# Optimization experiments

Hardware: AMD Instinct MI355X
Metric: run time of the kernel (lower is better)

## Reference

```python
import jax, jax.numpy as jnp
import numpy as np

# Hyperparameters matching the torch module instantiation
STRIDE = (2, 2, 2)
PADDING = (1, 1, 1)
OUTPUT_PADDING = (1, 1, 1)
DILATION = (2, 2, 2)
KERNEL = (3, 3, 3)


def setup_inputs() -> dict:
    key = jax.random.key(0)
    k1, k2, k3 = jax.random.split(key, 3)
    x = jax.random.normal(k1, (2, 64, 32, 32, 32), dtype=jnp.float32)
    # torch ConvTranspose3d weight layout: (C_in, C_out//groups, kD, kH, kW)
    weight = jax.random.normal(k2, (64, 32, 3, 3, 3), dtype=jnp.float32) * 0.05
    bias = jax.random.normal(k3, (32,), dtype=jnp.float32) * 0.05
    return {"x": x, "weight": weight, "bias": bias}


def reference(x, weight, bias):
    # Same math as the naive torch module: zero-insertion upsample by stride,
    # symmetric pad by dilation*(k-1)-padding, dense conv3d with the spatially
    # flipped weight at rhs dilation, trailing output_padding, then bias add.
    # lhs_dilation performs the zero-insertion implicitly (identical result).
    pad = tuple(max(0, d * (k - 1) - p)
                for d, k, p in zip(DILATION, KERNEL, PADDING))
    # (C_in, C_out, k,k,k) -> (C_out, C_in, k,k,k), flipped spatially
    w = jnp.flip(jnp.transpose(weight, (1, 0, 2, 3, 4)), axis=(2, 3, 4))
    out = jax.lax.conv_general_dilated(
        x, w,
        window_strides=(1, 1, 1),
        padding=[(p, p) for p in pad],
        lhs_dilation=STRIDE,
        rhs_dilation=DILATION,
        dimension_numbers=("NCDHW", "OIDHW", "NCDHW"),
    )
    opd, oph, opw = OUTPUT_PADDING
    out = jnp.pad(out, ((0, 0), (0, 0), (0, opd), (0, oph), (0, opw)))
    return out + bias[None, :, None, None, None]
```

## Files before the change

### kernel.cpp

```cpp
#include <hip/hip_runtime.h>


#define DOUT 66
#define PL (DOUT*DOUT)

typedef _Float16 half8 __attribute__((ext_vector_type(8)));
typedef float    floatx16 __attribute__((ext_vector_type(16)));

#define X16_N_F16  2228224
#define ROW_B      4352
#define ZSLAB_OFF  112640
#define X16_OFF    131072

#define PB_W    216
#define PB_X    512
#define PB_BA   579
#define PB_BB   561
#define PREP_GRID (PB_W + PB_X + PB_BA + PB_BB)

__global__ void __launch_bounds__(256) prep(
    const float* __restrict__ x, const float* __restrict__ w,
    const float* __restrict__ bias, _Float16* __restrict__ wA,
    _Float16* __restrict__ x16, uint4* __restrict__ zslab,
    float* __restrict__ out)
{
    const int tid = threadIdx.x;
    unsigned b = blockIdx.x;

    if (b < PB_W) {
        int o = b * 256 + tid;
        int j = o & 7;
        int tmp = o >> 3;
        int lane = tmp & 63;
        int g = tmp >> 6;
        int cc = g / 27, tap = g - cc * 27;
        int co = lane & 31, khalf = lane >> 5;
        int ci = cc * 16 + khalf * 8 + j;
        wA[o] = (_Float16)w[ci * 864 + co * 27 + tap];
        return;
    }
    b -= PB_W;
    if (b < PB_X) {
        const int id = b & 31;
        const int q2 = (b >> 5) & 7;
        const int n  = b >> 8;
        const int iw = tid & 31;
        const int cihalf = (tid >> 5) & 1;
        const int ihq = tid >> 6;
        const int ih = q2 * 4 + ihq;

        if (b == 0 && tid < 256) {
            zslab[2 * tid]     = make_uint4(0, 0, 0, 0);
            zslab[2 * tid + 1] = make_uint4(0, 0, 0, 0);
        }

        const float* xr = x + (size_t)n * 2097152 + (id * 32 + ih) * 32 + iw;
        _Float16* drow = x16 + (size_t)n * X16_N_F16 + (id * 32 + ih) * 2176;
        const int c0 = cihalf * 32;

        float f[32];
        #pragma unroll
        for (int j = 0; j < 32; ++j) f[j] = xr[(size_t)(c0 + j) * 32768];
        #pragma unroll
        for (int k = 0; k < 4; ++k) {
            unsigned pk[4];
            #pragma unroll
            for (int j = 0; j < 4; ++j)
                pk[j] = __builtin_bit_cast(unsigned,
                    __builtin_amdgcn_cvt_pkrtz(f[8 * k + 2 * j], f[8 * k + 2 * j + 1]));
            const int ccg = cihalf * 4 + k;
            *(uint4*)(drow + ccg * 272 + (iw + 1) * 8) =
                make_uint4(pk[0], pk[1], pk[2], pk[3]);
        }
        if (tid < 64) {
            const int ihq2 = tid >> 4;
            const int rem  = tid & 15;
            const int ccg  = rem >> 1, side = rem & 1;
            _Float16* hz = x16 + (size_t)n * X16_N_F16 +
                (id * 32 + q2 * 4 + ihq2) * 2176 + ccg * 272 + (side ? 264 : 0);
            *(uint4*)hz = make_uint4(0, 0, 0, 0);
        }
        return;
    }
    b -= PB_X;
    if (b < PB_BA) {
        const unsigned base = b * 4096u;
        #pragma unroll
        for (int j = 0; j < 16; ++j) {
            unsigned idx = base + j * 256u + tid;
            if (idx >= 2369952u) continue;
            unsigned pl = idx / 1089u;
            unsigned slot = idx - pl * 1089u;
            unsigned e  = pl % 34u;
            unsigned nc = pl / 34u;
            unsigned od = (e < 33u) ? 2u * e : 65u;
            float v = bias[nc & 31u];
            float4* p = (float4*)(out + ((size_t)nc * DOUT + od) * PL);
            p[slot] = make_float4(v, v, v, v);
        }
        return;
    }
    b -= PB_BA;
    {
        const unsigned base = b * 4096u;
        #pragma unroll
        for (int j = 0; j < 16; ++j) {
            unsigned idx = base + j * 256u + tid;
            unsigned slot = idx % 33u;
            unsigned t2   = idx / 33u;
            unsigned rr   = t2 % 34u;
            unsigned pln  = t2 / 34u;
            unsigned oh = (rr < 33u) ? 2u * rr : 65u;
            unsigned od = 2u * (pln & 31u) + 1u;
            unsigned nc = pln >> 5;
            float v = bias[nc & 31u];
            float2* p = (float2*)(out + ((size_t)nc * DOUT + od) * PL + oh * DOUT);
            p[slot] = make_float2(v, v);
        }
    }
}

__global__ void __launch_bounds__(256, 2) convt_mfma(
    const _Float16* __restrict__ x16, const _Float16* __restrict__ wA,
    const _Float16* __restrict__ zslab, const float* __restrict__ bias,
    float* __restrict__ out)
{
    __shared__ __align__(16) unsigned char xlds[78848];

    const int tid  = threadIdx.x;
    const int lane = tid & 63;
    const int wv   = tid >> 6;

    unsigned b = blockIdx.x;
    const unsigned xcd = b & 7u;
    const int n   = xcd & 1;
    const int dp  = (b >> 3) & 31;
    const int hq  = b >> 8;
    const int hpg = (int)(((xcd >> 1) << 1) | hq);
    const int hpb = hpg * 4;

    const char* xby = (const char*)(x16 + (size_t)n * X16_N_F16);
    const char* zby = (const char*)zslab;
    for (int m = wv; m < 77; m += 4) {
        int c = m * 64 + lane;
        int r = c / 272;
        int q = c - r * 272;
        const char* g;
        if (r < 18) {
            int idl = r / 6, ihl = r - idl * 6;
            int id = dp - 1 + idl, ih = hpb - 1 + ihl;
            bool v = ((unsigned)id < 32u) & ((unsigned)ih < 32u);
            g = v ? (xby + (id * 32 + ih) * ROW_B + q * 16) : (zby + q * 16);
        } else {
            g = zby;
        }
        __builtin_amdgcn_global_load_lds(
            (const __attribute__((address_space(1))) void*)g,
            (__attribute__((address_space(3))) void*)(xlds + m * 1024),
            16, 0, 0);
    }

    uint4 A[27];
    const _Float16* wl = wA + ((size_t)wv * 27 * 64 + lane) * 8;
    #pragma unroll
    for (int t = 0; t < 27; ++t) A[t] = *(const uint4*)(wl + t * 512);

    __syncthreads();

    const int wp    = lane & 31;
    const int khalf = lane >> 5;
    const int cbase = (2 * wv + khalf) * 544 + wp * 16;

    floatx16 acc[4] = {{}, {}, {}, {}};
    #pragma unroll
    for (int kd = 0; kd < 3; ++kd)
    #pragma unroll
    for (int kh = 0; kh < 3; ++kh)
    #pragma unroll
    for (int kw = 0; kw < 3; ++kw) {
        const int tap = (kd * 3 + kh) * 3 + kw;
        #pragma unroll
        for (int t = 0; t < 4; ++t) {
            const int row = (2 - kd) * 6 + (t + 2 - kh);
            const uint4* bp = (const uint4*)(xlds + row * ROW_B + cbase + (2 - kw) * 16);
            acc[t] = __builtin_amdgcn_mfma_f32_32x32x16_f16(
                __builtin_bit_cast(half8, A[tap]),
                __builtin_bit_cast(half8, *bp), acc[t], 0, 0, 0);
        }
    }

    __syncthreads();
    float* part = (float*)xlds;
    #pragma unroll
    for (int t = 0; t < 4; ++t) {
        if (t == wv) continue;
        #pragma unroll
        for (int r = 0; r < 16; ++r)
            part[((t * 4 + wv) * 16 + r) * 64 + lane] = acc[t][r];
    }
    __syncthreads();

    float s[16];
    #pragma unroll
    for (int r = 0; r < 16; ++r) s[r] = acc[wv][r];
    #pragma unroll
    for (int w2 = 0; w2 < 4; ++w2) {
        if (w2 == wv) continue;
        #pragma unroll
        for (int r = 0; r < 16; ++r)
            s[r] += part[((wv * 4 + w2) * 16 + r) * 64 + lane];
    }

    const int od = 2 * dp + 1;
    const int oh = 2 * (hpb + wv) + 1;
    #pragma unroll
    for (int r = 0; r < 16; ++r) {
        const int co = (r & 3) + 8 * (r >> 2) + 4 * khalf;
        const float bv = bias[co];
        float2* orow = (float2*)(out +
            ((size_t)(n * 32 + co) * DOUT + od) * PL + oh * DOUT);
        orow[wp] = make_float2(bv, s[r] + bv);
        if (wp == 31) orow[32] = make_float2(bv, bv);
    }
}

extern "C" void kernel_launch(void* const* d_in, const int* in_sizes, int n_in,
                              void* d_out, int out_size, void* d_ws, size_t ws_size,
                              hipStream_t stream) {
    const float* x    = (const float*)d_in[0];
    const float* wgt  = (const float*)d_in[1];
    const float* bias = (const float*)d_in[2];
    float* out = (float*)d_out;
    _Float16* wA    = (_Float16*)d_ws;
    uint4*    zslab = (uint4*)((char*)d_ws + ZSLAB_OFF);
    _Float16* x16   = (_Float16*)((char*)d_ws + X16_OFF);

    prep<<<PREP_GRID, 256, 0, stream>>>(x, wgt, bias, wA, x16, zslab, out);
    convt_mfma<<<512, 256, 0, stream>>>(x16, wA, (const _Float16*)zslab, bias, out);
}
```

Measured before the change: 118.0 us.

## Move bias-only output fill into conv kernel to overlap with MFMA work

Moves the bias-only plane fill (even od planes) out of the prep kernel into the conv kernel, interleaving fill blocks with conv blocks so the pure-store traffic overlaps with compute. The conv blocks now also write the even-oh rows of odd-od planes and the tail rows, which removes the second bias-fill pass. Prep becomes lighter and no longer waits on output stores, but conv blocks carry more store work and the LDS-heavy blocks now share the grid with fill blocks that allocate the same static shared memory.

```diff
diff --git a/kernel.cpp b/kernel.cpp
--- a/kernel.cpp
+++ b/kernel.cpp
@@ -14,15 +14,16 @@
 
 #define PB_W    216
 #define PB_X    512
-#define PB_BA   579
-#define PB_BB   561
-#define PREP_GRID (PB_W + PB_X + PB_BA + PB_BB)
+#define PREP_GRID (PB_W + PB_X)
+
+#define NB_CONV 512
+#define NB_BIAS 579
+#define CB_GRID (NB_CONV + NB_BIAS)
 
 __global__ void __launch_bounds__(256) prep(
     const float* __restrict__ x, const float* __restrict__ w,
-    const float* __restrict__ bias, _Float16* __restrict__ wA,
-    _Float16* __restrict__ x16, uint4* __restrict__ zslab,
-    float* __restrict__ out)
+    _Float16* __restrict__ wA, _Float16* __restrict__ x16,
+    uint4* __restrict__ zslab)
 {
     const int tid = threadIdx.x;
     unsigned b = blockIdx.x;
@@ -40,7 +41,7 @@
         return;
     }
     b -= PB_W;
-    if (b < PB_X) {
+    {
         const int id = b & 31;
         const int q2 = (b >> 5) & 7;
         const int n  = b >> 8;
@@ -49,7 +50,7 @@
         const int ihq = tid >> 6;
         const int ih = q2 * 4 + ihq;
 
-        if (b == 0 && tid < 256) {
+        if (b == 0) {
             zslab[2 * tid]     = make_uint4(0, 0, 0, 0);
             zslab[2 * tid + 1] = make_uint4(0, 0, 0, 0);
         }
@@ -80,17 +81,32 @@
                 (id * 32 + q2 * 4 + ihq2) * 2176 + ccg * 272 + (side ? 264 : 0);
             *(uint4*)hz = make_uint4(0, 0, 0, 0);
         }
-        return;
-    }
-    b -= PB_X;
-    if (b < PB_BA) {
-        const unsigned base = b * 4096u;
+    }
+}
+
+__global__ void __launch_bounds__(256, 2) convbias(
+    const _Float16* __restrict__ x16, const _Float16* __restrict__ wA,
+    const _Float16* __restrict__ zslab, const float* __restrict__ bias,
+    float* __restrict__ out)
+{
+    __shared__ __align__(16) unsigned char xlds[78848];
+
+    const int tid = threadIdx.x;
+    unsigned b = blockIdx.x;
+
+    bool is_conv;
+    unsigned idx;
+    if (b < 1024u) { is_conv = !(b & 1u); idx = b >> 1; }
+    else           { is_conv = false;     idx = 512u + (b - 1024u); }
+
+    if (!is_conv) {
+        const unsigned base = idx * 4096u;
         #pragma unroll
         for (int j = 0; j < 16; ++j) {
-            unsigned idx = base + j * 256u + tid;
-            if (idx >= 2369952u) continue;
-            unsigned pl = idx / 1089u;
-            unsigned slot = idx - pl * 1089u;
+            unsigned g = base + j * 256u + tid;
+            if (g >= 2369952u) continue;
+            unsigned pl = g / 1089u;
+            unsigned slot = g - pl * 1089u;
             unsigned e  = pl % 34u;
             unsigned nc = pl / 34u;
             unsigned od = (e < 33u) ? 2u * e : 65u;
@@ -100,42 +116,14 @@
         }
         return;
     }
-    b -= PB_BA;
-    {
-        const unsigned base = b * 4096u;
-        #pragma unroll
-        for (int j = 0; j < 16; ++j) {
-            unsigned idx = base + j * 256u + tid;
-            unsigned slot = idx % 33u;
-            unsigned t2   = idx / 33u;
-            unsigned rr   = t2 % 34u;
-            unsigned pln  = t2 / 34u;
-            unsigned oh = (rr < 33u) ? 2u * rr : 65u;
-            unsigned od = 2u * (pln & 31u) + 1u;
-            unsigned nc = pln >> 5;
-            float v = bias[nc & 31u];
-            float2* p = (float2*)(out + ((size_t)nc * DOUT + od) * PL + oh * DOUT);
-            p[slot] = make_float2(v, v);
-        }
-    }
-}
-
-__global__ void __launch_bounds__(256, 2) convt_mfma(
-    const _Float16* __restrict__ x16, const _Float16* __restrict__ wA,
-    const _Float16* __restrict__ zslab, const float* __restrict__ bias,
-    float* __restrict__ out)
-{
-    __shared__ __align__(16) unsigned char xlds[78848];
-
-    const int tid  = threadIdx.x;
+
     const int lane = tid & 63;
     const int wv   = tid >> 6;
 
-    unsigned b = blockIdx.x;
-    const unsigned xcd = b & 7u;
+    const unsigned xcd = idx & 7u;
     const int n   = xcd & 1;
-    const int dp  = (b >> 3) & 31;
-    const int hq  = b >> 8;
+    const int dp  = (idx >> 3) & 31;
+    const int hq  = idx >> 8;
     const int hpg = (int)(((xcd >> 1) << 1) | hq);
     const int hpb = hpg * 4;
 
@@ -212,15 +200,29 @@
     }
 
     const int od = 2 * dp + 1;
-    const int oh = 2 * (hpb + wv) + 1;
+    const int hp = hpb + wv;
+    const int oh_odd = 2 * hp + 1, oh_even = 2 * hp;
+    const bool tails = (hpg == 7) && (wv == 3);
     #pragma unroll
     for (int r = 0; r < 16; ++r) {
         const int co = (r & 3) + 8 * (r >> 2) + 4 * khalf;
         const float bv = bias[co];
-        float2* orow = (float2*)(out +
-            ((size_t)(n * 32 + co) * DOUT + od) * PL + oh * DOUT);
+        float* pbase = out + ((size_t)(n * 32 + co) * DOUT + od) * PL;
+        float2* orow = (float2*)(pbase + oh_odd * DOUT);
+        float2* erow = (float2*)(pbase + oh_even * DOUT);
         orow[wp] = make_float2(bv, s[r] + bv);
-        if (wp == 31) orow[32] = make_float2(bv, bv);
+        erow[wp] = make_float2(bv, bv);
+        if (wp == 31) {
+            orow[32] = make_float2(bv, bv);
+            erow[32] = make_float2(bv, bv);
+        }
+        if (tails) {
+            float2* t0 = (float2*)(pbase + 64 * DOUT);
+            float2* t1 = (float2*)(pbase + 65 * DOUT);
+            t0[wp] = make_float2(bv, bv);
+            t1[wp] = make_float2(bv, bv);
+            if (wp == 31) { t0[32] = make_float2(bv, bv); t1[32] = make_float2(bv, bv); }
+        }
     }
 }
 
@@ -235,6 +237,6 @@
     uint4*    zslab = (uint4*)((char*)d_ws + ZSLAB_OFF);
     _Float16* x16   = (_Float16*)((char*)d_ws + X16_OFF);
 
-    prep<<<PREP_GRID, 256, 0, stream>>>(x, wgt, bias, wA, x16, zslab, out);
-    convt_mfma<<<512, 256, 0, stream>>>(x16, wA, (const _Float16*)zslab, bias, out);
+    prep<<<PREP_GRID, 256, 0, stream>>>(x, wgt, wA, x16, zslab);
+    convbias<<<CB_GRID, 256, 0, stream>>>(x16, wA, (const _Float16*)zslab, bias, out);
 }
```

Measured after the change: 120.5 us. 2.1% more time.

## Halve conv tile height to raise occupancy and move bias-only row writes into conv kernel

Applied to the files above, without the earlier changes.

The conv kernel now covers 2 output rows per block instead of 4, launching 1024 blocks with smaller LDS (4 input rows per depth instead of 6) and a launch bound of 3 blocks per CU. The two idle waves in the epilogue write the bias-only even output rows of odd depth planes. This removes the second bias-fill phase from the prep kernel. The trade-off is more redundant halo loading per block and more partial-sum reduction traffic through LDS, in exchange for higher occupancy and less prep work.

```diff
diff --git a/kernel.cpp b/kernel.cpp
--- a/kernel.cpp
+++ b/kernel.cpp
@@ -14,9 +14,8 @@
 
 #define PB_W    216
 #define PB_X    512
-#define PB_BA   579
-#define PB_BB   561
-#define PREP_GRID (PB_W + PB_X + PB_BA + PB_BB)
+#define PB_B    579
+#define PREP_GRID (PB_W + PB_X + PB_B)
 
 __global__ void __launch_bounds__(256) prep(
     const float* __restrict__ x, const float* __restrict__ w,
@@ -49,7 +48,7 @@
         const int ihq = tid >> 6;
         const int ih = q2 * 4 + ihq;
 
-        if (b == 0 && tid < 256) {
+        if (b == 0) {
             zslab[2 * tid]     = make_uint4(0, 0, 0, 0);
             zslab[2 * tid + 1] = make_uint4(0, 0, 0, 0);
         }
@@ -83,14 +82,14 @@
         return;
     }
     b -= PB_X;
-    if (b < PB_BA) {
+    {
         const unsigned base = b * 4096u;
         #pragma unroll
         for (int j = 0; j < 16; ++j) {
-            unsigned idx = base + j * 256u + tid;
-            if (idx >= 2369952u) continue;
-            unsigned pl = idx / 1089u;
-            unsigned slot = idx - pl * 1089u;
+            unsigned g = base + j * 256u + tid;
+            if (g >= 2369952u) continue;
+            unsigned pl = g / 1089u;
+            unsigned slot = g - pl * 1089u;
             unsigned e  = pl % 34u;
             unsigned nc = pl / 34u;
             unsigned od = (e < 33u) ? 2u * e : 65u;
@@ -98,34 +97,15 @@
             float4* p = (float4*)(out + ((size_t)nc * DOUT + od) * PL);
             p[slot] = make_float4(v, v, v, v);
         }
-        return;
-    }
-    b -= PB_BA;
-    {
-        const unsigned base = b * 4096u;
-        #pragma unroll
-        for (int j = 0; j < 16; ++j) {
-            unsigned idx = base + j * 256u + tid;
-            unsigned slot = idx % 33u;
-            unsigned t2   = idx / 33u;
-            unsigned rr   = t2 % 34u;
-            unsigned pln  = t2 / 34u;
-            unsigned oh = (rr < 33u) ? 2u * rr : 65u;
-            unsigned od = 2u * (pln & 31u) + 1u;
-            unsigned nc = pln >> 5;
-            float v = bias[nc & 31u];
-            float2* p = (float2*)(out + ((size_t)nc * DOUT + od) * PL + oh * DOUT);
-            p[slot] = make_float2(v, v);
-        }
     }
 }
 
-__global__ void __launch_bounds__(256, 2) convt_mfma(
+__global__ void __launch_bounds__(256, 3) convt(
     const _Float16* __restrict__ x16, const _Float16* __restrict__ wA,
     const _Float16* __restrict__ zslab, const float* __restrict__ bias,
     float* __restrict__ out)
 {
-    __shared__ __align__(16) unsigned char xlds[78848];
+    __shared__ __align__(16) unsigned char xlds[52224];
 
     const int tid  = threadIdx.x;
     const int lane = tid & 63;
@@ -134,26 +114,23 @@
     unsigned b = blockIdx.x;
     const unsigned xcd = b & 7u;
     const int n   = xcd & 1;
-    const int dp  = (b >> 3) & 31;
-    const int hq  = b >> 8;
-    const int hpg = (int)(((xcd >> 1) << 1) | hq);
-    const int hpb = hpg * 4;
+    const unsigned rest = b >> 3;
+    const int dp  = rest & 31;
+    const int hq2 = rest >> 5;
+    const int hpg = (int)((xcd >> 1) * 4 + hq2);
+    const int hpb = hpg * 2;
 
     const char* xby = (const char*)(x16 + (size_t)n * X16_N_F16);
     const char* zby = (const char*)zslab;
-    for (int m = wv; m < 77; m += 4) {
+    for (int m = wv; m < 51; m += 4) {
         int c = m * 64 + lane;
-        int r = c / 272;
+        int r = c >> 8;
+        r = c / 272;
         int q = c - r * 272;
-        const char* g;
-        if (r < 18) {
-            int idl = r / 6, ihl = r - idl * 6;
-            int id = dp - 1 + idl, ih = hpb - 1 + ihl;
-            bool v = ((unsigned)id < 32u) & ((unsigned)ih < 32u);
-            g = v ? (xby + (id * 32 + ih) * ROW_B + q * 16) : (zby + q * 16);
-        } else {
-            g = zby;
-        }
+        int idl = r >> 2, ihl = r & 3;
+        int id = dp - 1 + idl, ih = hpb - 1 + ihl;
+        bool v = ((unsigned)id < 32u) & ((unsigned)ih < 32u);
+        const char* g = v ? (xby + (id * 32 + ih) * ROW_B + q * 16) : (zby + q * 16);
         __builtin_amdgcn_global_load_lds(
             (const __attribute__((address_space(1))) void*)g,
             (__attribute__((address_space(3))) void*)(xlds + m * 1024),
@@ -171,7 +148,7 @@
     const int khalf = lane >> 5;
     const int cbase = (2 * wv + khalf) * 544 + wp * 16;
 
-    floatx16 acc[4] = {{}, {}, {}, {}};
+    floatx16 acc0 = {}, acc1 = {};
     #pragma unroll
     for (int kd = 0; kd < 3; ++kd)
     #pragma unroll
@@ -179,48 +156,71 @@
     #pragma unroll
     for (int kw = 0; kw < 3; ++kw) {
         const int tap = (kd * 3 + kh) * 3 + kw;
-        #pragma unroll
-        for (int t = 0; t < 4; ++t) {
-            const int row = (2 - kd) * 6 + (t + 2 - kh);
-            const uint4* bp = (const uint4*)(xlds + row * ROW_B + cbase + (2 - kw) * 16);
-            acc[t] = __builtin_amdgcn_mfma_f32_32x32x16_f16(
-                __builtin_bit_cast(half8, A[tap]),
-                __builtin_bit_cast(half8, *bp), acc[t], 0, 0, 0);
-        }
+        const int row0 = (2 - kd) * 4 + (2 - kh);
+        const uint4* bp0 = (const uint4*)(xlds + row0 * ROW_B + cbase + (2 - kw) * 16);
+        acc0 = __builtin_amdgcn_mfma_f32_32x32x16_f16(
+            __builtin_bit_cast(half8, A[tap]),
+            __builtin_bit_cast(half8, bp0[0]), acc0, 0, 0, 0);
+        const uint4* bp1 = (const uint4*)((const char*)bp0 + ROW_B);
+        acc1 = __builtin_amdgcn_mfma_f32_32x32x16_f16(
+            __builtin_bit_cast(half8, A[tap]),
+            __builtin_bit_cast(half8, bp1[0]), acc1, 0, 0, 0);
     }
 
     __syncthreads();
     float* part = (float*)xlds;
-    #pragma unroll
-    for (int t = 0; t < 4; ++t) {
-        if (t == wv) continue;
+    if (wv != 0) {
         #pragma unroll
         for (int r = 0; r < 16; ++r)
-            part[((t * 4 + wv) * 16 + r) * 64 + lane] = acc[t][r];
+            part[((wv * 2 + 0) * 16 + r) * 64 + lane] = acc0[r];
+    }
+    if (wv != 1) {
+        #pragma unroll
+        for (int r = 0; r < 16; ++r)
+            part[((wv * 2 + 1) * 16 + r) * 64 + lane] = acc1[r];
     }
     __syncthreads();
 
-    float s[16];
-    #pragma unroll
-    for (int r = 0; r < 16; ++r) s[r] = acc[wv][r];
-    #pragma unroll
-    for (int w2 = 0; w2 < 4; ++w2) {
-        if (w2 == wv) continue;
-        #pragma unroll
-        for (int r = 0; r < 16; ++r)
-            s[r] += part[((wv * 4 + w2) * 16 + r) * 64 + lane];
-    }
-
     const int od = 2 * dp + 1;
-    const int oh = 2 * (hpb + wv) + 1;
-    #pragma unroll
-    for (int r = 0; r < 16; ++r) {
-        const int co = (r & 3) + 8 * (r >> 2) + 4 * khalf;
-        const float bv = bias[co];
-        float2* orow = (float2*)(out +
-            ((size_t)(n * 32 + co) * DOUT + od) * PL + oh * DOUT);
-        orow[wp] = make_float2(bv, s[r] + bv);
-        if (wp == 31) orow[32] = make_float2(bv, bv);
+    if (wv <= 1) {
+        float s[16];
+        #pragma unroll
+        for (int r = 0; r < 16; ++r) {
+            s[r] = (wv == 0) ? acc0[r] : acc1[r];
+            #pragma unroll
+            for (int w2 = 0; w2 < 4; ++w2) {
+                if (w2 == wv) continue;
+                s[r] += part[((w2 * 2 + wv) * 16 + r) * 64 + lane];
+            }
+        }
+        const int oh = 2 * (hpb + wv) + 1;
+        #pragma unroll
+        for (int r = 0; r < 16; ++r) {
+            const int co = (r & 3) + 8 * (r >> 2) + 4 * khalf;
+            const float bv = bias[co];
+            float2* orow = (float2*)(out +
+                ((size_t)(n * 32 + co) * DOUT + od) * PL + oh * DOUT);
+            orow[wp] = make_float2(bv, s[r] + bv);
+            if (wp == 31) orow[32] = make_float2(bv, bv);
+        }
+    } else {
+        const int oh = (wv == 2) ? 2 * hpb : 2 * hpb + 2;
+        const int oht = (wv == 2) ? 64 : 65;
+        const bool tails = (hpg == 15);
+        #pragma unroll
+        for (int r = 0; r < 16; ++r) {
+            const int co = (r & 3) + 8 * (r >> 2) + 4 * khalf;
+            const float bv = bias[co];
+            float* pbase = out + ((size_t)(n * 32 + co) * DOUT + od) * PL;
+            float2* erow = (float2*)(pbase + oh * DOUT);
+            erow[wp] = make_float2(bv, bv);
+            if (wp == 31) erow[32] = make_float2(bv, bv);
+            if (tails) {
+                float2* trow = (float2*)(pbase + oht * DOUT);
+                trow[wp] = make_float2(bv, bv);
+                if (wp == 31) trow[32] = make_float2(bv, bv);
+            }
+        }
     }
 }
 
@@ -236,5 +236,5 @@
     _Float16* x16   = (_Float16*)((char*)d_ws + X16_OFF);
 
     prep<<<PREP_GRID, 256, 0, stream>>>(x, wgt, bias, wA, x16, zslab, out);
-    convt_mfma<<<512, 256, 0, stream>>>(x16, wA, (const _Float16*)zslab, bias, out);
+    convt<<<1024, 256, 0, stream>>>(x16, wA, (const _Float16*)zslab, bias, out);
 }
```

Result: faster. 109.0 us (-7.6%).
